# Kernel tuning notes

Hardware: AMD Instinct MI355X
Metric: run time of the kernel (lower is better)

Reference implementation:

```python
import jax, jax.numpy as jnp
import numpy as np
import math

B, N, D = 1, 50000, 512  # batch (forced to 1 by the module's matmul shapes), nodes, embed_dim


def _uniform(key, shape, stdv):
    return jax.random.uniform(key, shape, minval=-stdv, maxval=stdv, dtype=jnp.float32)


def setup_inputs() -> dict:
    key = jax.random.key(0)
    ks = jax.random.split(key, 11)
    q = jax.random.normal(ks[0], (B, N, D), dtype=jnp.float32)
    l = jax.random.normal(ks[1], (B, 1, D), dtype=jnp.float32)
    context = jax.random.normal(ks[2], (B, 1, D), dtype=jnp.float32)
    g = jax.random.normal(ks[3], (B, 1, D), dtype=jnp.float32)
    mask = jax.random.randint(ks[4], (B, N), 0, 2, dtype=jnp.int32)
    mask = mask.at[:, 0].set(1)  # guarantee at least one feasible node
    random_net = jax.random.randint(ks[5], (B, 1), 0, N, dtype=jnp.int64)
    # learned parameters, uniform(-1/sqrt(fan), 1/sqrt(fan)) per init_parameters
    W_context = _uniform(ks[6], (1, 1, 2), 1.0 / math.sqrt(2))
    W_graph = _uniform(ks[7], (1, 1, 2), 1.0 / math.sqrt(2))
    W_query = _uniform(ks[8], (D, D), 1.0 / math.sqrt(D))
    W_key = _uniform(ks[9], (D, D), 1.0 / math.sqrt(D))
    return {
        "q": q, "l": l, "context": context, "g": g, "mask": mask,
        "is_random": 0, "random_net": random_net,
        "W_context": W_context, "W_graph": W_graph,
        "W_query": W_query, "W_key": W_key,
    }


def reference(q, l, context, g, mask, is_random, random_net,
              W_context, W_graph, W_query, W_key):
    batch_size, graph_size, input_dim = q.shape
    mask_copy = mask
    norm_factor = 1.0 / math.sqrt(input_dim)  # key_dim == embed_dim (n_heads=1)

    # context mixing: concat = W_context[0] @ [l; context]  -> (B,1,D)
    lc = jnp.concatenate([l, context], axis=1).reshape(-1, input_dim)      # (2B, D)
    concat = jnp.matmul(W_context[0], lc).reshape(batch_size, 1, input_dim)
    # graph mixing: g_context = W_graph[0] @ [g; concat]    -> (B,1,D)
    gc = jnp.concatenate([g, concat], axis=1).reshape(-1, input_dim)
    g_context = jnp.matmul(W_graph[0], gc).reshape(batch_size, 1, input_dim)

    Q = jnp.matmul(g_context.reshape(-1, input_dim), W_query).reshape(batch_size, 1, -1)
    K = jnp.matmul(q.reshape(-1, input_dim), W_key).reshape(batch_size, graph_size, -1)

    compat = jnp.tanh(norm_factor * jnp.einsum('bqk,bnk->bqn', Q, K)) * 10.0  # (B,1,N)
    maskf = mask.astype(jnp.float32)[:, None, :]
    compat = jnp.where(maskf <= 0.1, -jnp.inf, compat)

    softmax = jax.nn.softmax(compat, axis=2)
    log_softmax = jax.nn.log_softmax(compat, axis=2)

    if not is_random:  # static Python branch (is_random is a plain int)
        max_indx = jnp.argmax(softmax, axis=2)          # (B,1)
    else:
        max_indx = random_net

    rows = jnp.arange(batch_size)
    idx = max_indx[:, 0]
    q_max = q[rows, idx][:, None, :]                    # (B,1,D)
    attn_max = softmax[rows, 0, idx].reshape(batch_size, 1)
    log_attn_max = log_softmax[rows, 0, idx].reshape(batch_size, 1)
    return (q_max, attn_max, log_attn_max, concat, mask_copy, max_indx)
```

## Files before the change

kernel.cpp:

```cpp
#include <hip/hip_runtime.h>
#include <math.h>

#define DIM 512
#define NROWS 50000
#define NORM 0.04419417382415922f

#define QPART_BLOCKS 32
#define VK_BLOCKS 128
#define CP_BLOCKS 1024
#define CP_THREADS 256

#define OUT_ATTN 512
#define OUT_LOG  513
#define OUT_IDX  51026


__device__ inline float dot4(float4 a, float4 b, float acc) {
    acc = fmaf(a.x, b.x, acc);
    acc = fmaf(a.y, b.y, acc);
    acc = fmaf(a.z, b.z, acc);
    acc = fmaf(a.w, b.w, acc);
    return acc;
}

__device__ inline void sm_combine(float& m, float& s, int& idx,
                                  float m2, float s2, int idx2) {
    bool take2 = (m2 > m) || (m2 == m && idx2 < idx);
    float hm = take2 ? m2 : m;
    float hs = take2 ? s2 : s;
    int   hi = take2 ? idx2 : idx;
    float lm = take2 ? m : m2;
    float ls = take2 ? s : s2;
    if (lm > -INFINITY) hs = fmaf(ls, expf(lm - hm), hs);
    m = hm; s = hs; idx = hi;
}

__global__ __launch_bounds__(256) void qpart_kernel(
    const float* __restrict__ l, const float* __restrict__ ctx,
    const float* __restrict__ g, const float* __restrict__ Wc,
    const float* __restrict__ Wg, const float* __restrict__ Wq,
    float* __restrict__ qpart, float* __restrict__ out_concat) {
    __shared__ float gctx[DIM];
    int t = threadIdx.x;
    float wc0 = Wc[0], wc1 = Wc[1], wg0 = Wg[0], wg1 = Wg[1];
    for (int j = t; j < DIM; j += 256) {
        float cc = wc0 * l[j] + wc1 * ctx[j];
        if (blockIdx.x == 0) out_concat[j] = cc;
        gctx[j] = wg0 * g[j] + wg1 * cc;
    }
    __syncthreads();
    int d0 = blockIdx.x * 16;
    float acc0 = 0.f, acc1 = 0.f;
    for (int d = d0; d < d0 + 16; ++d) {
        float gd = gctx[d];
        acc0 = fmaf(gd, Wq[d * DIM + t], acc0);
        acc1 = fmaf(gd, Wq[d * DIM + t + 256], acc1);
    }
    qpart[blockIdx.x * DIM + t] = acc0;
    qpart[blockIdx.x * DIM + t + 256] = acc1;
}

__global__ __launch_bounds__(256) void v_kernel(
    const float* __restrict__ Wk, const float* __restrict__ qpart,
    float* __restrict__ v) {
    __shared__ __align__(16) float Q[DIM];
    int t = threadIdx.x;
    for (int j = t; j < DIM; j += 256) {
        float a = 0.f;
        for (int p = 0; p < QPART_BLOCKS; ++p) a += qpart[p * DIM + j];
        Q[j] = a;
    }
    __syncthreads();
    int lane = t & 63;
    int w = t >> 6;
    int r = blockIdx.x * 4 + w;
    const float4* row = (const float4*)(Wk + (size_t)r * DIM);
    const float4* qv = (const float4*)Q;
    float4 a0 = row[lane],      a1 = row[lane + 64];
    float4 b0 = qv[lane],       b1 = qv[lane + 64];
    float d = dot4(a1, b1, dot4(a0, b0, 0.f));
    #pragma unroll
    for (int off = 32; off > 0; off >>= 1) d += __shfl_xor(d, off);
    if (lane == 0) v[r] = d;
}

__global__ __launch_bounds__(CP_THREADS) void compat_kernel(
    const float* __restrict__ q, const int* __restrict__ mask,
    const float* __restrict__ v, float* __restrict__ compat,
    float* __restrict__ pm, float* __restrict__ ps, int* __restrict__ pidx,
    float* __restrict__ out_maskf) {
    int t = threadIdx.x;
    int gtid = blockIdx.x * CP_THREADS + t;
    int gsz = gridDim.x * CP_THREADS;
    for (int i = gtid; i < NROWS; i += gsz)
        out_maskf[i] = (float)mask[i];

    int lane = t & 63;
    int wid = gtid >> 6;
    int nw = gsz >> 6;

    const float4* vv = (const float4*)v;
    float4 b0 = vv[lane];
    float4 b1 = vv[lane + 64];

    float m = -INFINITY, s = 0.f;
    int idx = 0x7fffffff;

    for (int n = wid; n < NROWS; n += nw) {
        if (mask[n] == 0) {
            if (lane == 0) compat[n] = -INFINITY;
            continue;
        }
        const float4* row = (const float4*)(q + (size_t)n * DIM);
        float4 a0 = row[lane];
        float4 a1 = row[lane + 64];
        float d = dot4(a1, b1, dot4(a0, b0, 0.f));
        #pragma unroll
        for (int off = 32; off > 0; off >>= 1) d += __shfl_xor(d, off);
        float c = tanhf(NORM * d) * 10.0f;
        if (lane == 0) compat[n] = c;
        sm_combine(m, s, idx, c, 1.0f, n);
    }

    __shared__ float bm[CP_THREADS / 64], bs[CP_THREADS / 64];
    __shared__ int bidx[CP_THREADS / 64];
    int w = t >> 6;
    if (lane == 0) { bm[w] = m; bs[w] = s; bidx[w] = idx; }
    __syncthreads();
    if (t == 0) {
        float M = bm[0], S = bs[0];
        int I = bidx[0];
        for (int i = 1; i < CP_THREADS / 64; ++i)
            sm_combine(M, S, I, bm[i], bs[i], bidx[i]);
        pm[blockIdx.x] = M;
        ps[blockIdx.x] = S;
        pidx[blockIdx.x] = I;
    }
}

__global__ __launch_bounds__(512) void finalize_kernel(
    const float* __restrict__ q, const float* __restrict__ pm,
    const float* __restrict__ ps, const int* __restrict__ pidx,
    const float* __restrict__ compat, const int* __restrict__ is_random,
    const long long* __restrict__ rnet, float* __restrict__ out) {
    __shared__ float sm[512], ss[512];
    __shared__ int si[512];
    __shared__ int chosen;
    int t = threadIdx.x;
    float m = -INFINITY, s = 0.f;
    int idx = 0x7fffffff;
    for (int i = t; i < CP_BLOCKS; i += 512)
        sm_combine(m, s, idx, pm[i], ps[i], pidx[i]);
    sm[t] = m; ss[t] = s; si[t] = idx;
    __syncthreads();
    for (int off = 256; off > 0; off >>= 1) {
        if (t < off) {
            float M = sm[t], S = ss[t];
            int I = si[t];
            sm_combine(M, S, I, sm[t + off], ss[t + off], si[t + off]);
            sm[t] = M; ss[t] = S; si[t] = I;
        }
        __syncthreads();
    }
    if (t == 0) {
        float M = sm[0], S = ss[0];
        int ix = si[0];
        if (is_random[0] != 0) ix = (int)rnet[0];
        float c = compat[ix];
        out[OUT_ATTN] = expf(c - M) / S;
        out[OUT_LOG]  = (c - M) - logf(S);
        out[OUT_IDX]  = (float)ix;
        chosen = ix;
    }
    __syncthreads();
    out[t] = q[(size_t)chosen * DIM + t];
}

extern "C" void kernel_launch(void* const* d_in, const int* in_sizes, int n_in,
                              void* d_out, int out_size, void* d_ws, size_t ws_size,
                              hipStream_t stream) {
    const float*     q    = (const float*)d_in[0];
    const float*     l    = (const float*)d_in[1];
    const float*     ctx  = (const float*)d_in[2];
    const float*     g    = (const float*)d_in[3];
    const int*       mask = (const int*)d_in[4];
    const int*       isr  = (const int*)d_in[5];
    const long long* rnet = (const long long*)d_in[6];
    const float*     Wc   = (const float*)d_in[7];
    const float*     Wg   = (const float*)d_in[8];
    const float*     Wq   = (const float*)d_in[9];
    const float*     Wk   = (const float*)d_in[10];

    float* out = (float*)d_out;
    float* ws  = (float*)d_ws;
    float* qpart  = ws;
    float* v      = ws + 16384;
    float* pm     = ws + 16896;
    float* ps     = ws + 17920;
    int*   pidx   = (int*)(ws + 18944);
    float* compat = ws + 19968;

    qpart_kernel<<<QPART_BLOCKS, 256, 0, stream>>>(l, ctx, g, Wc, Wg, Wq, qpart, out + 514);
    v_kernel<<<VK_BLOCKS, 256, 0, stream>>>(Wk, qpart, v);
    compat_kernel<<<CP_BLOCKS, CP_THREADS, 0, stream>>>(q, mask, v, compat, pm, ps, pidx, out + 1026);
    finalize_kernel<<<1, 512, 0, stream>>>(q, pm, ps, pidx, compat, isr, rnet, out);
}
```

Before: 31.65 us.

## Fuse finalize into compat kernel via last-block atomic and drop compat buffer

The separate finalize kernel is folded into the compat kernel: each block publishes its partial softmax stats, increments an atomic counter, and the last block to finish performs the global reduction and writes the outputs. The per-row compat array is no longer stored; the chosen logit is taken from the max, or recomputed from q and v for the random index. The row loop now handles two rows per iteration and prefetches mask values for the next pair, giving more loads in flight. This removes one kernel launch and the compat writes, at the cost of a counter reset in qpart_kernel, threadfences, and a serial tail in the last block.

```diff
diff --git a/kernel.cpp b/kernel.cpp
--- a/kernel.cpp
+++ b/kernel.cpp
@@ -39,9 +39,11 @@
     const float* __restrict__ l, const float* __restrict__ ctx,
     const float* __restrict__ g, const float* __restrict__ Wc,
     const float* __restrict__ Wg, const float* __restrict__ Wq,
-    float* __restrict__ qpart, float* __restrict__ out_concat) {
+    float* __restrict__ qpart, float* __restrict__ out_concat,
+    unsigned* __restrict__ counter) {
     __shared__ float gctx[DIM];
     int t = threadIdx.x;
+    if (blockIdx.x == 0 && t == 0) *counter = 0u;
     float wc0 = Wc[0], wc1 = Wc[1], wg0 = Wg[0], wg1 = Wg[1];
     for (int j = t; j < DIM; j += 256) {
         float cc = wc0 * l[j] + wc1 * ctx[j];
@@ -86,12 +88,14 @@
 
 __global__ __launch_bounds__(CP_THREADS) void compat_kernel(
     const float* __restrict__ q, const int* __restrict__ mask,
-    const float* __restrict__ v, float* __restrict__ compat,
+    const float* __restrict__ v,
     float* __restrict__ pm, float* __restrict__ ps, int* __restrict__ pidx,
-    float* __restrict__ out_maskf) {
+    unsigned* __restrict__ counter, const int* __restrict__ is_random,
+    const long long* __restrict__ rnet, float* __restrict__ out) {
     int t = threadIdx.x;
     int gtid = blockIdx.x * CP_THREADS + t;
-    int gsz = gridDim.x * CP_THREADS;
+    int gsz = CP_BLOCKS * CP_THREADS;
+    float* out_maskf = out + 1026;
     for (int i = gtid; i < NROWS; i += gsz)
         out_maskf[i] = (float)mask[i];
 
@@ -106,20 +110,34 @@
     float m = -INFINITY, s = 0.f;
     int idx = 0x7fffffff;
 
-    for (int n = wid; n < NROWS; n += nw) {
-        if (mask[n] == 0) {
-            if (lane == 0) compat[n] = -INFINITY;
-            continue;
-        }
-        const float4* row = (const float4*)(q + (size_t)n * DIM);
-        float4 a0 = row[lane];
-        float4 a1 = row[lane + 64];
-        float d = dot4(a1, b1, dot4(a0, b0, 0.f));
+    int n = wid;
+    int mk1 = (n < NROWS) ? mask[n] : 0;
+    int mk2 = (n + nw < NROWS) ? mask[n + nw] : 0;
+    for (; n < NROWS; n += 2 * nw) {
+        int nn = n + 2 * nw;
+        int mk1n = (nn < NROWS) ? mask[nn] : 0;
+        int mk2n = (nn + nw < NROWS) ? mask[nn + nw] : 0;
+
+        float4 a0, a1, c0, c1;
+        if (mk1) {
+            const float4* r1 = (const float4*)(q + (size_t)n * DIM);
+            a0 = r1[lane]; a1 = r1[lane + 64];
+        }
+        if (mk2) {
+            const float4* r2 = (const float4*)(q + (size_t)(n + nw) * DIM);
+            c0 = r2[lane]; c1 = r2[lane + 64];
+        }
+        float d1 = 0.f, d2 = 0.f;
+        if (mk1) d1 = dot4(a1, b1, dot4(a0, b0, 0.f));
+        if (mk2) d2 = dot4(c1, b1, dot4(c0, b0, 0.f));
         #pragma unroll
-        for (int off = 32; off > 0; off >>= 1) d += __shfl_xor(d, off);
-        float c = tanhf(NORM * d) * 10.0f;
-        if (lane == 0) compat[n] = c;
-        sm_combine(m, s, idx, c, 1.0f, n);
+        for (int off = 32; off > 0; off >>= 1) {
+            d1 += __shfl_xor(d1, off);
+            d2 += __shfl_xor(d2, off);
+        }
+        if (mk1) sm_combine(m, s, idx, tanhf(NORM * d1) * 10.0f, 1.0f, n);
+        if (mk2) sm_combine(m, s, idx, tanhf(NORM * d2) * 10.0f, 1.0f, n + nw);
+        mk1 = mk1n; mk2 = mk2n;
     }
 
     __shared__ float bm[CP_THREADS / 64], bs[CP_THREADS / 64];
@@ -127,6 +145,8 @@
     int w = t >> 6;
     if (lane == 0) { bm[w] = m; bs[w] = s; bidx[w] = idx; }
     __syncthreads();
+
+    __shared__ int lastFlag;
     if (t == 0) {
         float M = bm[0], S = bs[0];
         int I = bidx[0];
@@ -135,45 +155,62 @@
         pm[blockIdx.x] = M;
         ps[blockIdx.x] = S;
         pidx[blockIdx.x] = I;
-    }
-}
-
-__global__ __launch_bounds__(512) void finalize_kernel(
-    const float* __restrict__ q, const float* __restrict__ pm,
-    const float* __restrict__ ps, const int* __restrict__ pidx,
-    const float* __restrict__ compat, const int* __restrict__ is_random,
-    const long long* __restrict__ rnet, float* __restrict__ out) {
-    __shared__ float sm[512], ss[512];
-    __shared__ int si[512];
-    __shared__ int chosen;
-    int t = threadIdx.x;
-    float m = -INFINITY, s = 0.f;
-    int idx = 0x7fffffff;
-    for (int i = t; i < CP_BLOCKS; i += 512)
-        sm_combine(m, s, idx, pm[i], ps[i], pidx[i]);
-    sm[t] = m; ss[t] = s; si[t] = idx;
-    __syncthreads();
-    for (int off = 256; off > 0; off >>= 1) {
+        __threadfence();
+        unsigned old = atomicAdd(counter, 1u);
+        lastFlag = (old == CP_BLOCKS - 1) ? 1 : 0;
+    }
+    __syncthreads();
+    if (!lastFlag) return;
+    __threadfence();
+
+    __shared__ float fm[CP_THREADS], fs[CP_THREADS];
+    __shared__ int fi[CP_THREADS];
+    float M = -INFINITY, S = 0.f;
+    int I = 0x7fffffff;
+    for (int i = t; i < CP_BLOCKS; i += CP_THREADS)
+        sm_combine(M, S, I, pm[i], ps[i], pidx[i]);
+    fm[t] = M; fs[t] = S; fi[t] = I;
+    __syncthreads();
+    for (int off = CP_THREADS / 2; off > 0; off >>= 1) {
         if (t < off) {
-            float M = sm[t], S = ss[t];
-            int I = si[t];
-            sm_combine(M, S, I, sm[t + off], ss[t + off], si[t + off]);
-            sm[t] = M; ss[t] = S; si[t] = I;
+            float M2 = fm[t], S2 = fs[t];
+            int I2 = fi[t];
+            sm_combine(M2, S2, I2, fm[t + off], fs[t + off], fi[t + off]);
+            fm[t] = M2; fs[t] = S2; fi[t] = I2;
         }
         __syncthreads();
     }
+    __shared__ int chosenIx, chosenRnd;
+    __shared__ float chosenM, chosenS;
     if (t == 0) {
-        float M = sm[0], S = ss[0];
-        int ix = si[0];
-        if (is_random[0] != 0) ix = (int)rnet[0];
-        float c = compat[ix];
-        out[OUT_ATTN] = expf(c - M) / S;
-        out[OUT_LOG]  = (c - M) - logf(S);
+        chosenRnd = is_random[0];
+        chosenIx = chosenRnd ? (int)rnet[0] : fi[0];
+        chosenM = fm[0];
+        chosenS = fs[0];
+    }
+    __syncthreads();
+    int ix = chosenIx;
+    float rv0 = q[(size_t)ix * DIM + t];
+    float rv1 = q[(size_t)ix * DIM + t + 256];
+    out[t] = rv0;
+    out[t + 256] = rv1;
+    fm[t] = fmaf(rv0, v[t], rv1 * v[t + 256]);
+    __syncthreads();
+    for (int off = CP_THREADS / 2; off > 0; off >>= 1) {
+        if (t < off) fm[t] += fm[t + off];
+        __syncthreads();
+    }
+    if (t == 0) {
+        float Mv = chosenM, Sv = chosenS;
+        float c;
+        if (chosenRnd)
+            c = mask[ix] ? tanhf(NORM * fm[0]) * 10.0f : -INFINITY;
+        else
+            c = Mv;
+        out[OUT_ATTN] = expf(c - Mv) / Sv;
+        out[OUT_LOG]  = (c - Mv) - logf(Sv);
         out[OUT_IDX]  = (float)ix;
-        chosen = ix;
-    }
-    __syncthreads();
-    out[t] = q[(size_t)chosen * DIM + t];
+    }
 }
 
 extern "C" void kernel_launch(void* const* d_in, const int* in_sizes, int n_in,
@@ -193,15 +230,14 @@
 
     float* out = (float*)d_out;
     float* ws  = (float*)d_ws;
-    float* qpart  = ws;
-    float* v      = ws + 16384;
-    float* pm     = ws + 16896;
-    float* ps     = ws + 17920;
-    int*   pidx   = (int*)(ws + 18944);
-    float* compat = ws + 19968;
-
-    qpart_kernel<<<QPART_BLOCKS, 256, 0, stream>>>(l, ctx, g, Wc, Wg, Wq, qpart, out + 514);
+    float*    qpart   = ws;
+    float*    v       = ws + 16384;
+    float*    pm      = ws + 16896;
+    float*    ps      = ws + 17920;
+    int*      pidx    = (int*)(ws + 18944);
+    unsigned* counter = (unsigned*)(ws + 19968);
+
+    qpart_kernel<<<QPART_BLOCKS, 256, 0, stream>>>(l, ctx, g, Wc, Wg, Wq, qpart, out + 514, counter);
     v_kernel<<<VK_BLOCKS, 256, 0, stream>>>(Wk, qpart, v);
-    compat_kernel<<<CP_BLOCKS, CP_THREADS, 0, stream>>>(q, mask, v, compat, pm, ps, pidx, out + 1026);
-    finalize_kernel<<<1, 512, 0, stream>>>(q, pm, ps, pidx, compat, isr, rnet, out);
-}
+    compat_kernel<<<CP_BLOCKS, CP_THREADS, 0, stream>>>(q, mask, v, pm, ps, pidx, counter, isr, rnet, out);
+}
```

After: 53.53 us. 69.1% more time.
